# Kernel tuning notes

Measured on AMD Instinct MI355X. Metric: run time of the kernel, lower is better.

The kernel has to match this reference:

```python
import jax, jax.numpy as jnp
import numpy as np

# db4 decomposition low-pass filter, pywt coefficient order
DEC_LO = np.array([-0.010597401784997278, 0.032883011666982945,
                   0.030841381835986965, -0.18703481171888114,
                   -0.02798376941698385, 0.6308807679295904,
                   0.7148465705525415, 0.23037781330885523], dtype=np.float32)
LEVEL = 5
B, C, L = 64, 64, 8192


def _qmf_hi(dec_lo):
    # pywt relation: dec_hi[n] = (-1)^(n+1) * dec_lo[F-1-n]
    F = dec_lo.shape[0]
    signs = jnp.where(jnp.arange(F) % 2 == 0, -1.0, 1.0).astype(dec_lo.dtype)
    return signs * dec_lo[::-1]


def _wavedec(x, dec_lo, dec_hi):
    # pywt.dwt(v, w, 'symmetric') == np.convolve(sym_pad(v, F-1), filt, 'valid')[1::2]
    # implemented as a stride-2 cross-correlation with the reversed filter.
    b, c, n = x.shape
    v = x.reshape(b * c, n)
    F = dec_lo.shape[0]
    # kernel: (out_ch=2 [lo, hi], in_ch=1, width=F); reversed => true convolution
    k = jnp.stack([dec_lo[::-1], dec_hi[::-1]])[:, None, :]
    details = []
    for _ in range(LEVEL):
        ext = jnp.pad(v, ((0, 0), (F - 1, F - 1)), mode='symmetric')[:, 1:]
        y = jax.lax.conv_general_dilated(ext[:, None, :], k,
                                         window_strides=(2,), padding='VALID')
        v = y[:, 0, :]           # approximation -> next level input
        details.append(y[:, 1, :])  # detail for this level (finest first)
    approx = v.reshape(b, c, -1)
    # pywt order: [cA_L, cD_L, ..., cD_1] -> coarsest detail first
    det = [d.reshape(b, c, -1) for d in reversed(details)]
    return (approx, *det)


def setup_inputs() -> dict:
    key = jax.random.key(0)
    x = jax.random.normal(key, (B, C, L), dtype=jnp.float32)
    dec_lo = jnp.asarray(DEC_LO)
    dec_hi = _qmf_hi(dec_lo)
    return {"x": x, "dec_lo": dec_lo, "dec_hi": dec_hi}


def reference(x, dec_lo, dec_hi):
    # Returns (cA_L, cD_L, cD_{L-1}, ..., cD_1), matching the torch module's
    # [approx_tensor, detail_tensors] flattened.
    return _wavedec(x, dec_lo, dec_hi)
```

## Files before the change

kernel.cpp:

```cpp
#include <hip/hip_runtime.h>


static constexpr int ROWS = 4096;
static constexpr int N0 = 8192;
static constexpr int L1n = 4099, L2n = 2053, L3n = 1030, L4n = 518, L5n = 262;
static constexpr size_t OFF_D5 = 1073152u;
static constexpr size_t OFF_D4 = 2146304u;
static constexpr size_t OFF_D3 = 4268032u;
static constexpr size_t OFF_D2 = 8486912u;
static constexpr size_t OFF_D1 = 16896000u;

typedef float f4 __attribute__((ext_vector_type(4)));
typedef f4 f4a __attribute__((aligned(4)));

template <bool LAST>
__device__ __forceinline__ void dwt_level(
    const float* __restrict__ src, int n, int m,
    const float* __restrict__ h, const float* __restrict__ g,
    float* __restrict__ adst, float* __restrict__ ddst, int tid)
{
    const int ngroups = (m + 3) >> 2;
    const int jmax = (n - 12) >> 3;
    for (int j = tid; j < ngroups; j += 256) {
        const int p0 = 4 * j;
        if (j >= 1 && j <= jmax && p0 + 3 < m) {
            const f4* __restrict__ s4 = reinterpret_cast<const f4*>(src + (8 * j - 8));
            f4 vv[5];
#pragma unroll
            for (int t = 0; t < 5; ++t) vv[t] = s4[t];
            float W[20];
#pragma unroll
            for (int i = 0; i < 20; ++i) W[i] = vv[i >> 2][i & 3];
            f4 aa, dd;
#pragma unroll
            for (int r = 0; r < 4; ++r) {
                float a = 0.f, d = 0.f;
#pragma unroll
                for (int q = 0; q < 8; ++q) {
                    const float v = W[2 * r + 9 - q];
                    a = fmaf(h[q], v, a);
                    d = fmaf(g[q], v, d);
                }
                aa[r] = a; dd[r] = d;
            }
            *reinterpret_cast<f4a*>(ddst + p0) = dd;
            if (LAST) *reinterpret_cast<f4a*>(adst + p0) = aa;
            else      *reinterpret_cast<f4*>(adst + p0) = aa;
        } else {
#pragma unroll 4
            for (int r = 0; r < 4; ++r) {
                const int pos = p0 + r;
                if (pos >= m) break;
                const int s0 = 2 * pos + 1;
                float a = 0.f, d = 0.f;
#pragma unroll
                for (int q = 0; q < 8; ++q) {
                    int s = s0 - q;
                    int idx = (s < 0) ? (-1 - s) : ((s >= n) ? (2 * n - 1 - s) : s);
                    const float v = src[idx];
                    a = fmaf(h[q], v, a);
                    d = fmaf(g[q], v, d);
                }
                ddst[pos] = d;
                adst[pos] = a;
            }
        }
    }
}

__global__ __launch_bounds__(256, 6)
void wavedec5_kernel(const float* __restrict__ x,
                     const float* __restrict__ dlo,
                     const float* __restrict__ dhi,
                     float* __restrict__ out)
{
    __shared__ __align__(16) float bufA[4100];
    __shared__ __align__(16) float bufB[2056];

    const int row = blockIdx.x;
    const int tid = threadIdx.x;

    float h[8], g[8];
#pragma unroll
    for (int i = 0; i < 8; ++i) { h[i] = dlo[i]; g[i] = dhi[i]; }

    const float* __restrict__ xr = x + (size_t)row * N0;

    dwt_level<false>(xr, N0, L1n, h, g, bufA,
                     out + OFF_D1 + (size_t)row * L1n, tid);
    __syncthreads();
    dwt_level<false>(bufA, L1n, L2n, h, g, bufB,
                     out + OFF_D2 + (size_t)row * L2n, tid);
    __syncthreads();
    dwt_level<false>(bufB, L2n, L3n, h, g, bufA,
                     out + OFF_D3 + (size_t)row * L3n, tid);
    __syncthreads();
    dwt_level<false>(bufA, L3n, L4n, h, g, bufB,
                     out + OFF_D4 + (size_t)row * L4n, tid);
    __syncthreads();
    dwt_level<true>(bufB, L4n, L5n, h, g,
                    out + (size_t)row * L5n,
                    out + OFF_D5 + (size_t)row * L5n, tid);
}

extern "C" void kernel_launch(void* const* d_in, const int* in_sizes, int n_in,
                              void* d_out, int out_size, void* d_ws, size_t ws_size,
                              hipStream_t stream) {
    const float* x   = (const float*)d_in[0];
    const float* dlo = (const float*)d_in[1];
    const float* dhi = (const float*)d_in[2];
    float* out = (float*)d_out;
    wavedec5_kernel<<<ROWS, 256, 0, stream>>>(x, dlo, dhi, out);
}
```

Measured before the change: 66.67 us.

## Process two rows per 512-thread block with float2 window loads and scalar stores

Each block now handles two rows with 512 threads, and each 256-thread half gets its own pair of LDS buffers. Input windows are loaded as eight float2 reads covering 16 floats instead of five float4 reads covering 20, which cuts redundant load bytes. Outputs are written as scalar stores rather than vector stores, since the output offsets are not 16-byte aligned. The risks are that scalar stores may raise the instruction count, and that the block-wide __syncthreads now couples two independent rows.

```diff
diff --git a/kernel.cpp b/kernel.cpp
--- a/kernel.cpp
+++ b/kernel.cpp
@@ -10,42 +10,42 @@
 static constexpr size_t OFF_D2 = 8486912u;
 static constexpr size_t OFF_D1 = 16896000u;
 
-typedef float f4 __attribute__((ext_vector_type(4)));
-typedef f4 f4a __attribute__((aligned(4)));
-
-template <bool LAST>
+template <int STRIDE, int UNROLL>
 __device__ __forceinline__ void dwt_level(
     const float* __restrict__ src, int n, int m,
     const float* __restrict__ h, const float* __restrict__ g,
     float* __restrict__ adst, float* __restrict__ ddst, int tid)
 {
     const int ngroups = (m + 3) >> 2;
-    const int jmax = (n - 12) >> 3;
-    for (int j = tid; j < ngroups; j += 256) {
+    const int jmax = (n - 10) >> 3;
+#pragma unroll UNROLL
+    for (int j = tid; j < ngroups; j += STRIDE) {
         const int p0 = 4 * j;
         if (j >= 1 && j <= jmax && p0 + 3 < m) {
-            const f4* __restrict__ s4 = reinterpret_cast<const f4*>(src + (8 * j - 8));
-            f4 vv[5];
+            const float2* __restrict__ s2 =
+                reinterpret_cast<const float2*>(src) + (4 * j - 3);
+            float w[16];
 #pragma unroll
-            for (int t = 0; t < 5; ++t) vv[t] = s4[t];
-            float W[20];
-#pragma unroll
-            for (int i = 0; i < 20; ++i) W[i] = vv[i >> 2][i & 3];
-            f4 aa, dd;
+            for (int t = 0; t < 8; ++t) {
+                const float2 v = s2[t];
+                w[2 * t] = v.x; w[2 * t + 1] = v.y;
+            }
+            float aa[4], dd[4];
 #pragma unroll
             for (int r = 0; r < 4; ++r) {
                 float a = 0.f, d = 0.f;
 #pragma unroll
                 for (int q = 0; q < 8; ++q) {
-                    const float v = W[2 * r + 9 - q];
+                    const float v = w[2 * r + 7 - q];
                     a = fmaf(h[q], v, a);
                     d = fmaf(g[q], v, d);
                 }
                 aa[r] = a; dd[r] = d;
             }
-            *reinterpret_cast<f4a*>(ddst + p0) = dd;
-            if (LAST) *reinterpret_cast<f4a*>(adst + p0) = aa;
-            else      *reinterpret_cast<f4*>(adst + p0) = aa;
+#pragma unroll
+            for (int r = 0; r < 4; ++r) ddst[p0 + r] = dd[r];
+#pragma unroll
+            for (int r = 0; r < 4; ++r) adst[p0 + r] = aa[r];
         } else {
 #pragma unroll 4
             for (int r = 0; r < 4; ++r) {
@@ -68,39 +68,42 @@
     }
 }
 
-__global__ __launch_bounds__(256, 6)
+__global__ __launch_bounds__(512, 3)
 void wavedec5_kernel(const float* __restrict__ x,
                      const float* __restrict__ dlo,
                      const float* __restrict__ dhi,
                      float* __restrict__ out)
 {
-    __shared__ __align__(16) float bufA[4100];
-    __shared__ __align__(16) float bufB[2056];
+    __shared__ __align__(16) float bufA[2][4100];
+    __shared__ __align__(16) float bufB[2][2056];
 
-    const int row = blockIdx.x;
-    const int tid = threadIdx.x;
+    const int half = threadIdx.x >> 8;
+    const int tid  = threadIdx.x & 255;
+    const int row  = (blockIdx.x << 1) + half;
 
     float h[8], g[8];
 #pragma unroll
     for (int i = 0; i < 8; ++i) { h[i] = dlo[i]; g[i] = dhi[i]; }
 
     const float* __restrict__ xr = x + (size_t)row * N0;
+    float* __restrict__ bA = bufA[half];
+    float* __restrict__ bB = bufB[half];
 
-    dwt_level<false>(xr, N0, L1n, h, g, bufA,
-                     out + OFF_D1 + (size_t)row * L1n, tid);
+    dwt_level<256, 2>(xr, N0, L1n, h, g, bA,
+                      out + OFF_D1 + (size_t)row * L1n, tid);
     __syncthreads();
-    dwt_level<false>(bufA, L1n, L2n, h, g, bufB,
-                     out + OFF_D2 + (size_t)row * L2n, tid);
+    dwt_level<256, 1>(bA, L1n, L2n, h, g, bB,
+                      out + OFF_D2 + (size_t)row * L2n, tid);
     __syncthreads();
-    dwt_level<false>(bufB, L2n, L3n, h, g, bufA,
-                     out + OFF_D3 + (size_t)row * L3n, tid);
+    dwt_level<256, 1>(bB, L2n, L3n, h, g, bA,
+                      out + OFF_D3 + (size_t)row * L3n, tid);
     __syncthreads();
-    dwt_level<false>(bufA, L3n, L4n, h, g, bufB,
-                     out + OFF_D4 + (size_t)row * L4n, tid);
+    dwt_level<256, 1>(bA, L3n, L4n, h, g, bB,
+                      out + OFF_D4 + (size_t)row * L4n, tid);
     __syncthreads();
-    dwt_level<true>(bufB, L4n, L5n, h, g,
-                    out + (size_t)row * L5n,
-                    out + OFF_D5 + (size_t)row * L5n, tid);
+    dwt_level<256, 1>(bB, L4n, L5n, h, g,
+                      out + (size_t)row * L5n,
+                      out + OFF_D5 + (size_t)row * L5n, tid);
 }
 
 extern "C" void kernel_launch(void* const* d_in, const int* in_sizes, int n_in,
@@ -110,5 +113,5 @@
     const float* dlo = (const float*)d_in[1];
     const float* dhi = (const float*)d_in[2];
     float* out = (float*)d_out;
-    wavedec5_kernel<<<ROWS, 256, 0, stream>>>(x, dlo, dhi, out);
+    wavedec5_kernel<<<ROWS / 2, 512, 0, stream>>>(x, dlo, dhi, out);
 }
```

Result: faster. 63.85 us (-4.2%).

## Software-pipeline DWT window loads and use nontemporal global stores

Applied to the files above, without the earlier changes.

Each thread now prefetches the next iteration's 16-float input window (as float2 loads from a tighter 14-float-aligned span) into registers while computing the current one. Output detail and final approximation writes become scalar nontemporal stores instead of 16-byte vector stores. The aim is to hide global/LDS load latency and reduce cache pollution from streaming outputs. The cost is more registers for the double buffer and split scalar stores, which may lower occupancy or store efficiency.

```diff
diff --git a/kernel.cpp b/kernel.cpp
--- a/kernel.cpp
+++ b/kernel.cpp
@@ -10,8 +10,22 @@
 static constexpr size_t OFF_D2 = 8486912u;
 static constexpr size_t OFF_D1 = 16896000u;
 
-typedef float f4 __attribute__((ext_vector_type(4)));
-typedef f4 f4a __attribute__((aligned(4)));
+__device__ __forceinline__ float refl_load(const float* __restrict__ s, int idx, int n) {
+    int i = (idx < 0) ? (-1 - idx) : ((idx >= n) ? (2 * n - 1 - idx) : idx);
+    return s[i];
+}
+
+template <typename SRC>
+__device__ __forceinline__ void load_window(const SRC* __restrict__ src,
+                                            int j, int jmax, float* __restrict__ w) {
+    int jb = j < 1 ? 1 : (j > jmax ? jmax : j);
+    const float2* __restrict__ s2 = reinterpret_cast<const float2*>(src) + (4 * jb - 3);
+#pragma unroll
+    for (int t = 0; t < 8; ++t) {
+        const float2 v = s2[t];
+        w[2 * t] = v.x; w[2 * t + 1] = v.y;
+    }
+}
 
 template <bool LAST>
 __device__ __forceinline__ void dwt_level(
@@ -20,32 +34,40 @@
     float* __restrict__ adst, float* __restrict__ ddst, int tid)
 {
     const int ngroups = (m + 3) >> 2;
-    const int jmax = (n - 12) >> 3;
-    for (int j = tid; j < ngroups; j += 256) {
+    const int jmax = (n - 10) >> 3;
+
+    float wc[16], wn[16];
+    int j = tid;
+    if (j < ngroups) load_window(src, j, jmax, wc);
+    while (j < ngroups) {
+        const int jn = j + 256;
+        if (jn < ngroups) load_window(src, jn, jmax, wn);
+
         const int p0 = 4 * j;
         if (j >= 1 && j <= jmax && p0 + 3 < m) {
-            const f4* __restrict__ s4 = reinterpret_cast<const f4*>(src + (8 * j - 8));
-            f4 vv[5];
-#pragma unroll
-            for (int t = 0; t < 5; ++t) vv[t] = s4[t];
-            float W[20];
-#pragma unroll
-            for (int i = 0; i < 20; ++i) W[i] = vv[i >> 2][i & 3];
-            f4 aa, dd;
+            float aa[4], dd[4];
 #pragma unroll
             for (int r = 0; r < 4; ++r) {
                 float a = 0.f, d = 0.f;
 #pragma unroll
                 for (int q = 0; q < 8; ++q) {
-                    const float v = W[2 * r + 9 - q];
+                    const float v = wc[2 * r + 7 - q];
                     a = fmaf(h[q], v, a);
                     d = fmaf(g[q], v, d);
                 }
                 aa[r] = a; dd[r] = d;
             }
-            *reinterpret_cast<f4a*>(ddst + p0) = dd;
-            if (LAST) *reinterpret_cast<f4a*>(adst + p0) = aa;
-            else      *reinterpret_cast<f4*>(adst + p0) = aa;
+#pragma unroll
+            for (int r = 0; r < 4; ++r)
+                __builtin_nontemporal_store(dd[r], ddst + p0 + r);
+            if (LAST) {
+#pragma unroll
+                for (int r = 0; r < 4; ++r)
+                    __builtin_nontemporal_store(aa[r], adst + p0 + r);
+            } else {
+#pragma unroll
+                for (int r = 0; r < 4; ++r) adst[p0 + r] = aa[r];
+            }
         } else {
 #pragma unroll 4
             for (int r = 0; r < 4; ++r) {
@@ -55,9 +77,7 @@
                 float a = 0.f, d = 0.f;
 #pragma unroll
                 for (int q = 0; q < 8; ++q) {
-                    int s = s0 - q;
-                    int idx = (s < 0) ? (-1 - s) : ((s >= n) ? (2 * n - 1 - s) : s);
-                    const float v = src[idx];
+                    const float v = refl_load(src, s0 - q, n);
                     a = fmaf(h[q], v, a);
                     d = fmaf(g[q], v, d);
                 }
@@ -65,6 +85,9 @@
                 adst[pos] = a;
             }
         }
+        j = jn;
+#pragma unroll
+        for (int t = 0; t < 16; ++t) wc[t] = wn[t];
     }
 }
 
```

Measured after the change: 62.00 us. -7.0%, faster.
